# Kernel optimization log

Measured on AMD Instinct MI355X. Metric: run time of the kernel, lower is better.

Reference implementation:

```python
import jax, jax.numpy as jnp
import numpy as np

HEAD_NUM = 16
MASK_FILL = 100000.0  # source uses +1e5 on masked entries (not -inf)


def setup_inputs() -> dict:
    key = jax.random.key(0)
    k1, k2, k3, k4, k5 = jax.random.split(key, 5)
    B, S, E = 2, 2048, 1024
    scale = 0.02
    return {
        "x": jax.random.normal(k1, (B, S, E), dtype=jnp.float32),
        "W_atten": jax.random.normal(k2, (E, 3 * E), dtype=jnp.float32) * scale,
        "b_atten": jax.random.normal(k3, (3 * E,), dtype=jnp.float32) * scale,
        "W_proj": jax.random.normal(k4, (E, E), dtype=jnp.float32) * scale,
        "b_proj": jax.random.normal(k5, (E,), dtype=jnp.float32) * scale,
    }


def reference(x, W_atten, b_atten, W_proj, b_proj):
    B, S, E = x.shape
    H = HEAD_NUM
    hd = E // H
    # QKV projection: [B, S, 3E]
    qkv = x @ W_atten + b_atten
    # reshape [B, S, H, 3*hd] -> [B, H, S, 3*hd], chunk into q,k,v [B,H,S,hd]
    qkv = jnp.transpose(qkv.reshape(B, S, H, 3 * hd), (0, 2, 1, 3))
    q, k, v = jnp.split(qkv, 3, axis=-1)
    # raw scores, NO 1/sqrt(dk) scaling (faithful to source)
    w = jnp.einsum("bhqd,bhkd->bhqk", q, k)
    # causal mask applied as w*mask + (1-mask)*1e5 (faithful to source)
    mask = jnp.tril(jnp.ones((S, S), dtype=w.dtype))
    w = w * mask + (1.0 - mask) * MASK_FILL
    # softmax over dim=1 == HEAD axis (faithful to source quirk)
    w = jax.nn.softmax(w, axis=1)
    # attn_drop: identity in eval mode
    a = jnp.einsum("bhqk,bhkd->bhqd", w, v)  # [B,H,S,hd]
    a = jnp.transpose(a, (0, 2, 1, 3)).reshape(B, S, E)
    h = a @ W_proj + b_proj
    # resi_drop: identity in eval mode
    return h
```

## Files before the change

### kernel.cpp

```cpp
#include <hip/hip_runtime.h>

#define DI __device__ __forceinline__

typedef __attribute__((ext_vector_type(8))) short s16x8;
typedef __attribute__((ext_vector_type(4))) short s16x4;
typedef __attribute__((ext_vector_type(4))) float f32x4;

DI unsigned short f2bf(float f){
  unsigned u = __float_as_uint(f);
  u = (u + 0x7FFFu + ((u >> 16) & 1u)) >> 16;
  return (unsigned short)u;
}
DI float bf2f(unsigned short h){
  return __uint_as_float(((unsigned)h) << 16);
}

DI void gll16(const void* g, void* l){
  __builtin_amdgcn_global_load_lds((const __attribute__((address_space(1))) void*)g,
                                   (__attribute__((address_space(3))) void*)l, 16, 0, 0);
}

__global__ void cvt_kernel(const float* __restrict__ in, unsigned short* __restrict__ out, int n8){
  int i = blockIdx.x * blockDim.x + threadIdx.x;
  if (i >= n8) return;
  const float4* p = (const float4*)in + (size_t)i * 2;
  float4 a = p[0], b = p[1];
  s16x8 o;
  o[0] = (short)f2bf(a.x); o[1] = (short)f2bf(a.y); o[2] = (short)f2bf(a.z); o[3] = (short)f2bf(a.w);
  o[4] = (short)f2bf(b.x); o[5] = (short)f2bf(b.y); o[6] = (short)f2bf(b.z); o[7] = (short)f2bf(b.w);
  ((s16x8*)out)[i] = o;
}

__global__ void transpose_cvt(const float* __restrict__ in, unsigned short* __restrict__ out, int R, int C){
  __shared__ float t[32][33];
  int c0 = blockIdx.x * 32, r0 = blockIdx.y * 32;
  int tx = threadIdx.x, ty = threadIdx.y;
  #pragma unroll
  for (int i = 0; i < 4; i++)
    t[ty + i*8][tx] = in[(size_t)(r0 + ty + i*8) * C + c0 + tx];
  __syncthreads();
  #pragma unroll
  for (int i = 0; i < 4; i++)
    out[(size_t)(c0 + ty + i*8) * R + r0 + tx] = f2bf(t[tx][ty + i*8]);
}

template<int MODE>
__global__ void gemm_kernel(const unsigned short* __restrict__ A,
                            const unsigned short* __restrict__ Wt,
                            const float* __restrict__ bias,
                            int N,
                            unsigned short* __restrict__ qb,
                            unsigned short* __restrict__ kb,
                            unsigned short* __restrict__ vt,
                            float* __restrict__ out)
{
  const int K = 1024;
  __shared__ unsigned short As[128 * 72];
  __shared__ unsigned short Bs[128 * 72];
  int m0 = blockIdx.y * 128, n0 = blockIdx.x * 128;
  int tid = threadIdx.x;
  int lane = tid & 63, wid = tid >> 6;
  int wm = (wid >> 1) * 64, wn = (wid & 1) * 64;
  int row_l = lane & 15, kgrp = lane >> 4;

  f32x4 acc[4][4];
  #pragma unroll
  for (int i = 0; i < 4; i++)
    #pragma unroll
    for (int j = 0; j < 4; j++)
      acc[i][j] = (f32x4){0.f, 0.f, 0.f, 0.f};

  for (int k0 = 0; k0 < K; k0 += 64){
    #pragma unroll
    for (int i = 0; i < 4; i++){
      int cid = tid + i * 256;
      int r = cid >> 3, c = (cid & 7) * 8;
      *(s16x8*)&As[r * 72 + c] = *(const s16x8*)&A [(size_t)(m0 + r) * K + k0 + c];
      *(s16x8*)&Bs[r * 72 + c] = *(const s16x8*)&Wt[(size_t)(n0 + r) * K + k0 + c];
    }
    __syncthreads();
    #pragma unroll
    for (int kc = 0; kc < 2; kc++){
      s16x8 af[4], bfr[4];
      #pragma unroll
      for (int mi = 0; mi < 4; mi++)
        af[mi] = *(const s16x8*)&As[(wm + mi*16 + row_l) * 72 + kc*32 + kgrp*8];
      #pragma unroll
      for (int ni = 0; ni < 4; ni++)
        bfr[ni] = *(const s16x8*)&Bs[(wn + ni*16 + row_l) * 72 + kc*32 + kgrp*8];
      #pragma unroll
      for (int mi = 0; mi < 4; mi++)
        #pragma unroll
        for (int ni = 0; ni < 4; ni++)
          acc[mi][ni] = __builtin_amdgcn_mfma_f32_16x16x32_bf16(af[mi], bfr[ni], acc[mi][ni], 0, 0, 0);
    }
    __syncthreads();
  }

  #pragma unroll
  for (int mi = 0; mi < 4; mi++){
    #pragma unroll
    for (int ni = 0; ni < 4; ni++){
      #pragma unroll
      for (int j = 0; j < 4; j++){
        int gr = m0 + wm + mi*16 + kgrp*4 + j;
        int gc = n0 + wn + ni*16 + row_l;
        float v = acc[mi][ni][j] + bias[gc];
        if (MODE == 0){
          int h = gc / 192, cc = gc % 192;
          int b = gr >> 11, s = gr & 2047;
          unsigned short bv = f2bf(v);
          if (cc < 64){
            qb[(size_t)gr * 1024 + h*64 + cc] = bv;
          } else if (cc < 128){
            int d = cc - 64; int kt = s >> 6, kk = s & 63;
            kb[(size_t)((b*16 + h)*32 + kt) * 4096 + ((kk*64 + d) ^ ((kk & 7) << 3))] = bv;
          } else {
            int d = cc - 128; int kt = s >> 6, kk = s & 63;
            vt[(size_t)((b*16 + h)*32 + kt) * 4096 + ((d*64 + kk) ^ ((d & 7) << 3))] = bv;
          }
        } else {
          out[(size_t)gr * N + gc] = v;
        }
      }
    }
  }
}

__global__ void sufv_kernel(const unsigned short* __restrict__ vt, float* __restrict__ sufv){
  __shared__ float tot[4][64];
  int bh = blockIdx.x;
  int tid = threadIdx.x;
  int tq = tid >> 6, d = tid & 63;
  const unsigned short* base = vt + (size_t)bh * 32 * 4096;
  float s[8];
  float run = 0.f;
  for (int j = 7; j >= 0; j--){
    int t = tq*8 + j;
    float rs = 0.f;
    #pragma unroll
    for (int c = 0; c < 8; c++){
      int idx = (d*64 + c*8) ^ ((d & 7) << 3);
      s16x8 v = *(const s16x8*)&base[(size_t)t*4096 + idx];
      #pragma unroll
      for (int e = 0; e < 8; e++) rs += bf2f((unsigned short)v[e]);
    }
    run += rs; s[j] = run;
  }
  tot[tq][d] = run;
  __syncthreads();
  float carry = 0.f;
  for (int t2 = tq+1; t2 < 4; t2++) carry += tot[t2][d];
  #pragma unroll
  for (int j = 0; j < 8; j++)
    sufv[((size_t)bh*33 + tq*8 + j)*64 + d] = s[j] + carry;
  if (tid < 64) sufv[((size_t)bh*33 + 32)*64 + tid] = 0.f;
}

__launch_bounds__(256)
__global__ void dpass_kernel(const unsigned short* __restrict__ qbuf,
                             const unsigned short* __restrict__ kb,
                             float* __restrict__ invDT)
{
  __shared__ unsigned short Kst[2][4096];
  int blk = blockIdx.x;
  int b = blk / 528, t = blk % 528;
  int qt = (int)((sqrtf(8.f*t + 1.f) - 1.f) * 0.5f);
  while ((qt+1)*(qt+2)/2 <= t) qt++;
  while (qt*(qt+1)/2 > t) qt--;
  int kt = t - qt*(qt+1)/2;

  int tid = threadIdx.x, lane = tid & 63, w = tid >> 6;
  int row_l = lane & 15, kgrp = lane >> 4;

  const unsigned short* ktb = kb + ((size_t)(b*16)*32 + kt) * 4096;

  auto stage = [&](int h, int buf){
    const unsigned short* src = ktb + (size_t)h * 32 * 4096;
    #pragma unroll
    for (int c = 0; c < 2; c++)
      gll16(src + (w*128 + c*64 + lane)*8, (void*)(&Kst[buf][0] + w*1024 + c*512));
  };

  stage(0, 0);

  f32x4 esum[4];
  #pragma unroll
  for (int ks = 0; ks < 4; ks++) esum[ks] = (f32x4){0.f,0.f,0.f,0.f};

  const unsigned short* qrow_p = qbuf + (size_t)(b*2048 + qt*64 + w*16 + row_l) * 1024;
  s16x8 qf0 = *(const s16x8*)&qrow_p[kgrp*8];
  s16x8 qf1 = *(const s16x8*)&qrow_p[32 + kgrp*8];

  for (int h = 0; h < 16; h++){
    int buf = h & 1;
    s16x8 qn0, qn1;
    if (h < 15){
      qn0 = *(const s16x8*)&qrow_p[(h+1)*64 + kgrp*8];
      qn1 = *(const s16x8*)&qrow_p[(h+1)*64 + 32 + kgrp*8];
      stage(h+1, buf ^ 1);
    }
    __builtin_amdgcn_sched_barrier(0);
    if (h < 15) asm volatile("s_waitcnt vmcnt(4)" ::: "memory");
    else        asm volatile("s_waitcnt vmcnt(0)" ::: "memory");
    __builtin_amdgcn_sched_barrier(0);
    __builtin_amdgcn_s_barrier();
    __builtin_amdgcn_sched_barrier(0);

    #pragma unroll
    for (int ks = 0; ks < 4; ks++){
      int row = ks*16 + row_l;
      int e0 = (row*64 + kgrp*8) ^ ((row & 7) << 3);
      int e1 = (row*64 + 32 + kgrp*8) ^ ((row & 7) << 3);
      s16x8 a0 = *(const s16x8*)&Kst[buf][e0];
      s16x8 a1 = *(const s16x8*)&Kst[buf][e1];
      f32x4 sc = __builtin_amdgcn_mfma_f32_16x16x32_bf16(a0, qf0, (f32x4){0.f,0.f,0.f,0.f}, 0, 0, 0);
      sc = __builtin_amdgcn_mfma_f32_16x16x32_bf16(a1, qf1, sc, 0, 0, 0);
      #pragma unroll
      for (int j = 0; j < 4; j++) esum[ks][j] += __expf(sc[j]);
    }
    __builtin_amdgcn_sched_barrier(0);
    __builtin_amdgcn_s_barrier();
    if (h < 15){ qf0 = qn0; qf1 = qn1; }
  }

  int qcol = qt*64 + w*16 + row_l;
  #pragma unroll
  for (int ks = 0; ks < 4; ks++)
    #pragma unroll
    for (int j = 0; j < 4; j++){
      int key = kt*64 + ks*16 + kgrp*4 + j;
      invDT[(size_t)b*4194304 + (size_t)key*2048 + qcol] = 1.f / esum[ks][j];
    }
}

__launch_bounds__(256)
__global__ void pv_kernel(const unsigned short* __restrict__ qbuf,
                          const unsigned short* __restrict__ kb,
                          const unsigned short* __restrict__ vt,
                          const float* __restrict__ invDT,
                          const float* __restrict__ sufv,
                          unsigned short* __restrict__ ab,
                          float* __restrict__ pb)
{
  __shared__ unsigned short Kst[2][4096];
  __shared__ unsigned short Vst[2][4096];
  __shared__ unsigned short Ws[4][16*72];

  int blk = blockIdx.x;
  int b = blk >> 9;
  int r = blk & 511;
  int h = r >> 5;
  int r2 = r & 31;
  int i = r2 >> 1, half = r2 & 1;
  int qsm = i, qbig = 31 - i;

  int tid = threadIdx.x, lane = tid & 63, w = tid >> 6;
  int row_l = lane & 15, kgrp = lane >> 4;

  const unsigned short* KT = kb + (size_t)((b*16 + h)*32) * 4096;
  const unsigned short* VT = vt + (size_t)((b*16 + h)*32) * 4096;
  const float* invB = invDT + (size_t)b * 4194304;

  auto stage = [&](int kt, int par){
    #pragma unroll
    for (int c = 0; c < 2; c++){
      gll16(KT + (size_t)kt*4096 + (w*128 + c*64 + lane)*8, (void*)(&Kst[par][0] + w*1024 + c*512));
      gll16(VT + (size_t)kt*4096 + (w*128 + c*64 + lane)*8, (void*)(&Vst[par][0] + w*1024 + c*512));
    }
  };

  auto run = [&](int qt, int k0t, int k1t, int mode){
    int q0 = qt * 64;
    int qv = q0 + w*16 + row_l;
    const unsigned short* qrow_p = qbuf + (size_t)(b*2048 + qv) * 1024 + h*64;
    s16x8 qf0 = *(const s16x8*)&qrow_p[kgrp*8];
    s16x8 qf1 = *(const s16x8*)&qrow_p[32 + kgrp*8];

    f32x4 pv[4];
    #pragma unroll
    for (int d = 0; d < 4; d++) pv[d] = (f32x4){0.f,0.f,0.f,0.f};

    stage(k0t, 0);

    for (int kt = k0t; kt < k1t; kt++){
      int par = (kt - k0t) & 1;
      float invd[4][4];
      #pragma unroll
      for (int ks = 0; ks < 4; ks++)
        #pragma unroll
        for (int j = 0; j < 4; j++){
          int key = kt*64 + ks*16 + kgrp*4 + j;
          invd[ks][j] = invB[(size_t)key*2048 + qv];
        }
      bool has_next = (kt + 1 < k1t);
      if (has_next) stage(kt+1, par ^ 1);
      __builtin_amdgcn_sched_barrier(0);
      if (has_next) asm volatile("s_waitcnt vmcnt(20)" ::: "memory");
      else          asm volatile("s_waitcnt vmcnt(16)" ::: "memory");
      __builtin_amdgcn_sched_barrier(0);
      __builtin_amdgcn_s_barrier();
      __builtin_amdgcn_sched_barrier(0);

      f32x4 sc[4];
      #pragma unroll
      for (int ks = 0; ks < 4; ks++){
        int row = ks*16 + row_l;
        int e0 = (row*64 + kgrp*8) ^ ((row & 7) << 3);
        int e1 = (row*64 + 32 + kgrp*8) ^ ((row & 7) << 3);
        s16x8 a0 = *(const s16x8*)&Kst[par][e0];
        s16x8 a1 = *(const s16x8*)&Kst[par][e1];
        sc[ks] = __builtin_amdgcn_mfma_f32_16x16x32_bf16(a0, qf0, (f32x4){0.f,0.f,0.f,0.f}, 0, 0, 0);
        sc[ks] = __builtin_amdgcn_mfma_f32_16x16x32_bf16(a1, qf1, sc[ks], 0, 0, 0);
      }
      #pragma unroll
      for (int ks = 0; ks < 4; ks++){
        #pragma unroll
        for (int j = 0; j < 4; j++){
          int key = kt*64 + ks*16 + kgrp*4 + j;
          float e = __expf(sc[ks][j]);
          sc[ks][j] = (key > qv) ? 0.0625f : e * invd[ks][j];
        }
        s16x4 pk;
        pk[0] = (short)f2bf(sc[ks][0]); pk[1] = (short)f2bf(sc[ks][1]);
        pk[2] = (short)f2bf(sc[ks][2]); pk[3] = (short)f2bf(sc[ks][3]);
        *(s16x4*)&Ws[w][row_l*72 + ks*16 + kgrp*4] = pk;
      }
      #pragma unroll
      for (int kc = 0; kc < 2; kc++){
        s16x8 af = *(const s16x8*)&Ws[w][row_l*72 + kc*32 + kgrp*8];
        #pragma unroll
        for (int dq = 0; dq < 4; dq++){
          int row = dq*16 + row_l;
          int ev = (row*64 + kc*32 + kgrp*8) ^ ((row & 7) << 3);
          s16x8 vf = *(const s16x8*)&Vst[par][ev];
          pv[dq] = __builtin_amdgcn_mfma_f32_16x16x32_bf16(af, vf, pv[dq], 0, 0, 0);
        }
      }
      __builtin_amdgcn_sched_barrier(0);
      __builtin_amdgcn_s_barrier();
    }

    if (mode == 0){
      int tsuf = qt + 1;
      #pragma unroll
      for (int dq = 0; dq < 4; dq++){
        int d = dq*16 + row_l;
        float suf = sufv[((size_t)(b*16 + h)*33 + tsuf)*64 + d];
        #pragma unroll
        for (int j = 0; j < 4; j++){
          int qo = q0 + w*16 + kgrp*4 + j;
          ab[(size_t)(b*2048 + qo)*1024 + h*64 + d] = f2bf(pv[dq][j] + 0.0625f * suf);
        }
      }
    } else {
      float* pr = pb + ((size_t)((b*16 + h)*16 + i)*2 + (mode - 1)) * 4096;
      #pragma unroll
      for (int dq = 0; dq < 4; dq++){
        int d = dq*16 + row_l;
        #pragma unroll
        for (int j = 0; j < 4; j++)
          pr[(w*16 + kgrp*4 + j)*64 + d] = pv[dq][j];
      }
    }
  };

  if (half == 0){
    run(qsm, 0, i + 1, 0);
    run(qbig, 0, 16 - i, 1);
  } else {
    run(qbig, 16 - i, 32 - i, 2);
  }
}

__global__ void reduce_kernel(const float* __restrict__ pb,
                              const float* __restrict__ sufv,
                              unsigned short* __restrict__ ab)
{
  int blk = blockIdx.x;
  int b = blk >> 8, rr = blk & 255;
  int h = rr >> 4, i = rr & 15;
  int qbig = 31 - i, tsuf = 32 - i;
  int t = threadIdx.x;
  int q = t >> 2, dbase = (t & 3) * 16;
  const float* p0 = pb + ((size_t)((b*16 + h)*16 + i)*2 + 0)*4096 + q*64 + dbase;
  const float* p1 = p0 + 4096;
  const float* sf = sufv + ((size_t)(b*16 + h)*33 + tsuf)*64 + dbase;
  unsigned short* op = ab + (size_t)(b*2048 + qbig*64 + q)*1024 + h*64 + dbase;
  #pragma unroll
  for (int e = 0; e < 4; e++){
    float4 a = *(const float4*)(p0 + e*4);
    float4 bb = *(const float4*)(p1 + e*4);
    float4 s = *(const float4*)(sf + e*4);
    unsigned short o[4];
    o[0] = f2bf(a.x + bb.x + 0.0625f * s.x);
    o[1] = f2bf(a.y + bb.y + 0.0625f * s.y);
    o[2] = f2bf(a.z + bb.z + 0.0625f * s.z);
    o[3] = f2bf(a.w + bb.w + 0.0625f * s.w);
    *(s16x4*)(op + e*4) = *(s16x4*)o;
  }
}

extern "C" void kernel_launch(void* const* d_in, const int* in_sizes, int n_in,
                              void* d_out, int out_size, void* d_ws, size_t ws_size,
                              hipStream_t stream) {
  (void)in_sizes; (void)n_in; (void)out_size; (void)ws_size;
  const float* x  = (const float*)d_in[0];
  const float* Wa = (const float*)d_in[1];
  const float* ba = (const float*)d_in[2];
  const float* Wp = (const float*)d_in[3];
  const float* bp = (const float*)d_in[4];
  float* out = (float*)d_out;

  char* ws = (char*)d_ws;
  size_t off = 0;
  auto alloc = [&](size_t bytes) -> void* {
    void* p = ws + off;
    off += (bytes + 255) & ~(size_t)255;
    return p;
  };
  float* pbuf          = (float*)alloc((size_t)16*1024*1024);
  unsigned short* xb   = (unsigned short*)((char*)pbuf);
  unsigned short* WaT  = (unsigned short*)((char*)pbuf + (size_t)4096*1024*2);
  unsigned short* WpT  = (unsigned short*)alloc((size_t)1024*1024*2);
  unsigned short* qbuf = (unsigned short*)alloc((size_t)4096*1024*2);
  unsigned short* ktile= (unsigned short*)alloc((size_t)4096*1024*2);
  unsigned short* vtile= (unsigned short*)alloc((size_t)4096*1024*2);
  unsigned short* abuf = (unsigned short*)alloc((size_t)4096*1024*2);
  float* invDT         = (float*)alloc((size_t)2*2048*2048*4);
  float* sufv          = (float*)alloc((size_t)32*33*64*4);

  cvt_kernel<<<2048, 256, 0, stream>>>(x, xb, 4096*1024/8);
  transpose_cvt<<<dim3(3072/32, 1024/32), dim3(32, 8), 0, stream>>>(Wa, WaT, 1024, 3072);
  transpose_cvt<<<dim3(1024/32, 1024/32), dim3(32, 8), 0, stream>>>(Wp, WpT, 1024, 1024);

  gemm_kernel<0><<<dim3(24, 32), 256, 0, stream>>>(xb, WaT, ba, 3072, qbuf, ktile, vtile, nullptr);

  sufv_kernel<<<32, 256, 0, stream>>>(vtile, sufv);

  dpass_kernel<<<1056, 256, 0, stream>>>(qbuf, ktile, invDT);

  pv_kernel<<<1024, 256, 0, stream>>>(qbuf, ktile, vtile, invDT, sufv, abuf, pbuf);

  reduce_kernel<<<512, 256, 0, stream>>>(pbuf, sufv, abuf);

  gemm_kernel<1><<<dim3(8, 32), 256, 0, stream>>>(abuf, WpT, bp, 1024, nullptr, nullptr, nullptr, out);
}
```

Measured before the change: 177.8 us.

## Deepen K/V prefetch, use direct-to-LDS GEMM loads, and transpose the inverse-denominator layout

The GEMM now loads tiles with global_load_lds into XOR-swizzled unpadded LDS, instead of staging them through registers. The dpass and pv kernels move from double to quad buffering with a prefetch distance of two tiles, which lets them drop the trailing barrier in each iteration. The inverse-denominator buffer is stored query-major, so dpass writes it and pv reads it as float4 vectors, and pv prefetches the next tile's values. The pv kernel also uses v_cvt_pk_bf16_f32 for packing and dynamic shared memory. These changes aim to hide global latency and cut strided scalar traffic, at the cost of more LDS use and hand-tuned vmcnt counts that must stay exact.

Result: no change. 177.7 us (-0.1%).

```diff
diff --git a/kernel.cpp b/kernel.cpp
--- a/kernel.cpp
+++ b/kernel.cpp
@@ -45,6 +45,7 @@
 }
 
 template<int MODE>
+__launch_bounds__(256)
 __global__ void gemm_kernel(const unsigned short* __restrict__ A,
                             const unsigned short* __restrict__ Wt,
                             const float* __restrict__ bias,
@@ -55,13 +56,33 @@
                             float* __restrict__ out)
 {
   const int K = 1024;
-  __shared__ unsigned short As[128 * 72];
-  __shared__ unsigned short Bs[128 * 72];
+  __shared__ unsigned short As[128 * 64];
+  __shared__ unsigned short Bs[128 * 64];
   int m0 = blockIdx.y * 128, n0 = blockIdx.x * 128;
   int tid = threadIdx.x;
-  int lane = tid & 63, wid = tid >> 6;
-  int wm = (wid >> 1) * 64, wn = (wid & 1) * 64;
+  int lane = tid & 63, w = tid >> 6;
   int row_l = lane & 15, kgrp = lane >> 4;
+  int wm = (w >> 1) * 64, wn = (w & 1) * 64;
+
+  const unsigned short* asrc[4];
+  const unsigned short* bsrc[4];
+  int ldso[4];
+  int chunk = (lane & 7) ^ (lane >> 3);
+  #pragma unroll
+  for (int c4 = 0; c4 < 4; c4++){
+    int r = c4*32 + w*8 + (lane >> 3);
+    asrc[c4] = A  + (size_t)(m0 + r) * K + chunk*8;
+    bsrc[c4] = Wt + (size_t)(n0 + r) * K + chunk*8;
+    ldso[c4] = (c4*32 + w*8) * 64;
+  }
+  int eA[4], eB[4];
+  #pragma unroll
+  for (int i = 0; i < 4; i++){
+    int ra = wm + i*16 + row_l;
+    eA[i] = (ra*64 + kgrp*8) ^ ((ra & 7) << 3);
+    int rb = wn + i*16 + row_l;
+    eB[i] = (rb*64 + kgrp*8) ^ ((rb & 7) << 3);
+  }
 
   f32x4 acc[4][4];
   #pragma unroll
@@ -72,11 +93,9 @@
 
   for (int k0 = 0; k0 < K; k0 += 64){
     #pragma unroll
-    for (int i = 0; i < 4; i++){
-      int cid = tid + i * 256;
-      int r = cid >> 3, c = (cid & 7) * 8;
-      *(s16x8*)&As[r * 72 + c] = *(const s16x8*)&A [(size_t)(m0 + r) * K + k0 + c];
-      *(s16x8*)&Bs[r * 72 + c] = *(const s16x8*)&Wt[(size_t)(n0 + r) * K + k0 + c];
+    for (int c4 = 0; c4 < 4; c4++){
+      gll16(asrc[c4] + k0, (void*)(As + ldso[c4]));
+      gll16(bsrc[c4] + k0, (void*)(Bs + ldso[c4]));
     }
     __syncthreads();
     #pragma unroll
@@ -84,10 +103,10 @@
       s16x8 af[4], bfr[4];
       #pragma unroll
       for (int mi = 0; mi < 4; mi++)
-        af[mi] = *(const s16x8*)&As[(wm + mi*16 + row_l) * 72 + kc*32 + kgrp*8];
+        af[mi] = *(const s16x8*)&As[eA[mi] ^ (kc*32)];
       #pragma unroll
       for (int ni = 0; ni < 4; ni++)
-        bfr[ni] = *(const s16x8*)&Bs[(wn + ni*16 + row_l) * 72 + kc*32 + kgrp*8];
+        bfr[ni] = *(const s16x8*)&Bs[eB[ni] ^ (kc*32)];
       #pragma unroll
       for (int mi = 0; mi < 4; mi++)
         #pragma unroll
@@ -160,9 +179,9 @@
 __launch_bounds__(256)
 __global__ void dpass_kernel(const unsigned short* __restrict__ qbuf,
                              const unsigned short* __restrict__ kb,
-                             float* __restrict__ invDT)
+                             float* __restrict__ invDQ)
 {
-  __shared__ unsigned short Kst[2][4096];
+  __shared__ unsigned short Kst[4][4096];
   int blk = blockIdx.x;
   int b = blk / 528, t = blk % 528;
   int qt = (int)((sqrtf(8.f*t + 1.f) - 1.f) * 0.5f);
@@ -174,15 +193,23 @@
   int row_l = lane & 15, kgrp = lane >> 4;
 
   const unsigned short* ktb = kb + ((size_t)(b*16)*32 + kt) * 4096;
-
-  auto stage = [&](int h, int buf){
-    const unsigned short* src = ktb + (size_t)h * 32 * 4096;
-    #pragma unroll
-    for (int c = 0; c < 2; c++)
-      gll16(src + (w*128 + c*64 + lane)*8, (void*)(&Kst[buf][0] + w*1024 + c*512));
+  int sgoff = (w*128 + lane)*8;
+
+  auto stage = [&](int hh, int buf){
+    const unsigned short* src = ktb + (size_t)hh * 131072;
+    gll16(src + sgoff,       (void*)(&Kst[buf][0] + w*1024));
+    gll16(src + sgoff + 512, (void*)(&Kst[buf][0] + w*1024 + 512));
   };
 
+  int e0[4];
+  #pragma unroll
+  for (int ks = 0; ks < 4; ks++){
+    int row = ks*16 + row_l;
+    e0[ks] = (row*64 + kgrp*8) ^ ((row & 7) << 3);
+  }
+
   stage(0, 0);
+  stage(1, 1);
 
   f32x4 esum[4];
   #pragma unroll
@@ -193,59 +220,57 @@
   s16x8 qf1 = *(const s16x8*)&qrow_p[32 + kgrp*8];
 
   for (int h = 0; h < 16; h++){
-    int buf = h & 1;
     s16x8 qn0, qn1;
     if (h < 15){
       qn0 = *(const s16x8*)&qrow_p[(h+1)*64 + kgrp*8];
       qn1 = *(const s16x8*)&qrow_p[(h+1)*64 + 32 + kgrp*8];
-      stage(h+1, buf ^ 1);
-    }
+    }
+    if (h + 2 < 16) stage(h+2, (h+2) & 3);
     __builtin_amdgcn_sched_barrier(0);
-    if (h < 15) asm volatile("s_waitcnt vmcnt(4)" ::: "memory");
-    else        asm volatile("s_waitcnt vmcnt(0)" ::: "memory");
+    if (h < 14)      asm volatile("s_waitcnt vmcnt(8)" ::: "memory");
+    else if (h < 15) asm volatile("s_waitcnt vmcnt(6)" ::: "memory");
+    else             asm volatile("s_waitcnt vmcnt(2)" ::: "memory");
     __builtin_amdgcn_sched_barrier(0);
     __builtin_amdgcn_s_barrier();
     __builtin_amdgcn_sched_barrier(0);
 
+    const unsigned short* kl = &Kst[h & 3][0];
     #pragma unroll
     for (int ks = 0; ks < 4; ks++){
-      int row = ks*16 + row_l;
-      int e0 = (row*64 + kgrp*8) ^ ((row & 7) << 3);
-      int e1 = (row*64 + 32 + kgrp*8) ^ ((row & 7) << 3);
-      s16x8 a0 = *(const s16x8*)&Kst[buf][e0];
-      s16x8 a1 = *(const s16x8*)&Kst[buf][e1];
+      s16x8 a0 = *(const s16x8*)&kl[e0[ks]];
+      s16x8 a1 = *(const s16x8*)&kl[e0[ks] ^ 32];
       f32x4 sc = __builtin_amdgcn_mfma_f32_16x16x32_bf16(a0, qf0, (f32x4){0.f,0.f,0.f,0.f}, 0, 0, 0);
       sc = __builtin_amdgcn_mfma_f32_16x16x32_bf16(a1, qf1, sc, 0, 0, 0);
       #pragma unroll
       for (int j = 0; j < 4; j++) esum[ks][j] += __expf(sc[j]);
     }
-    __builtin_amdgcn_sched_barrier(0);
-    __builtin_amdgcn_s_barrier();
     if (h < 15){ qf0 = qn0; qf1 = qn1; }
   }
 
   int qcol = qt*64 + w*16 + row_l;
-  #pragma unroll
-  for (int ks = 0; ks < 4; ks++)
-    #pragma unroll
-    for (int j = 0; j < 4; j++){
-      int key = kt*64 + ks*16 + kgrp*4 + j;
-      invDT[(size_t)b*4194304 + (size_t)key*2048 + qcol] = 1.f / esum[ks][j];
-    }
+  float* dst = invDQ + (size_t)b*4194304 + (size_t)qcol*2048 + kt*64 + kgrp*4;
+  #pragma unroll
+  for (int ks = 0; ks < 4; ks++){
+    f32x4 rv;
+    #pragma unroll
+    for (int j = 0; j < 4; j++) rv[j] = 1.f / esum[ks][j];
+    *(f32x4*)&dst[ks*16] = rv;
+  }
 }
 
 __launch_bounds__(256)
 __global__ void pv_kernel(const unsigned short* __restrict__ qbuf,
                           const unsigned short* __restrict__ kb,
                           const unsigned short* __restrict__ vt,
-                          const float* __restrict__ invDT,
+                          const float* __restrict__ invDQ,
                           const float* __restrict__ sufv,
                           unsigned short* __restrict__ ab,
                           float* __restrict__ pb)
 {
-  __shared__ unsigned short Kst[2][4096];
-  __shared__ unsigned short Vst[2][4096];
-  __shared__ unsigned short Ws[4][16*72];
+  extern __shared__ unsigned short lds[];
+  unsigned short* KstB = lds;
+  unsigned short* VstB = lds + 16384;
+  unsigned short* WsB  = lds + 32768;
 
   int blk = blockIdx.x;
   int b = blk >> 9;
@@ -260,14 +285,21 @@
 
   const unsigned short* KT = kb + (size_t)((b*16 + h)*32) * 4096;
   const unsigned short* VT = vt + (size_t)((b*16 + h)*32) * 4096;
-  const float* invB = invDT + (size_t)b * 4194304;
-
-  auto stage = [&](int kt, int par){
-    #pragma unroll
-    for (int c = 0; c < 2; c++){
-      gll16(KT + (size_t)kt*4096 + (w*128 + c*64 + lane)*8, (void*)(&Kst[par][0] + w*1024 + c*512));
-      gll16(VT + (size_t)kt*4096 + (w*128 + c*64 + lane)*8, (void*)(&Vst[par][0] + w*1024 + c*512));
-    }
+  int sgoff = (w*128 + lane)*8;
+  unsigned short* Wsw = WsB + w*1152;
+
+  int eK[4];
+  #pragma unroll
+  for (int ks = 0; ks < 4; ks++){
+    int row = ks*16 + row_l;
+    eK[ks] = (row*64 + kgrp*8) ^ ((row & 7) << 3);
+  }
+
+  auto stage = [&](int kt, int buf){
+    gll16(KT + (size_t)kt*4096 + sgoff,       (void*)(KstB + buf*4096 + w*1024));
+    gll16(KT + (size_t)kt*4096 + sgoff + 512, (void*)(KstB + buf*4096 + w*1024 + 512));
+    gll16(VT + (size_t)kt*4096 + sgoff,       (void*)(VstB + buf*4096 + w*1024));
+    gll16(VT + (size_t)kt*4096 + sgoff + 512, (void*)(VstB + buf*4096 + w*1024 + 512));
   };
 
   auto run = [&](int qt, int k0t, int k1t, int mode){
@@ -276,69 +308,69 @@
     const unsigned short* qrow_p = qbuf + (size_t)(b*2048 + qv) * 1024 + h*64;
     s16x8 qf0 = *(const s16x8*)&qrow_p[kgrp*8];
     s16x8 qf1 = *(const s16x8*)&qrow_p[32 + kgrp*8];
-
-    f32x4 pv[4];
-    #pragma unroll
-    for (int d = 0; d < 4; d++) pv[d] = (f32x4){0.f,0.f,0.f,0.f};
+    const float* ivrow = invDQ + (size_t)b*4194304 + (size_t)qv*2048 + kgrp*4;
+
+    f32x4 pvv[4];
+    #pragma unroll
+    for (int d = 0; d < 4; d++) pvv[d] = (f32x4){0.f,0.f,0.f,0.f};
 
     stage(k0t, 0);
+    f32x4 inxt[4];
+    #pragma unroll
+    for (int ks = 0; ks < 4; ks++) inxt[ks] = *(const f32x4*)&ivrow[k0t*64 + ks*16];
+    if (k0t + 1 < k1t) stage(k0t+1, 1);
 
     for (int kt = k0t; kt < k1t; kt++){
-      int par = (kt - k0t) & 1;
-      float invd[4][4];
-      #pragma unroll
-      for (int ks = 0; ks < 4; ks++)
-        #pragma unroll
-        for (int j = 0; j < 4; j++){
-          int key = kt*64 + ks*16 + kgrp*4 + j;
-          invd[ks][j] = invB[(size_t)key*2048 + qv];
-        }
-      bool has_next = (kt + 1 < k1t);
-      if (has_next) stage(kt+1, par ^ 1);
+      int par = (kt - k0t) & 3;
+      f32x4 icur[4];
+      #pragma unroll
+      for (int ks = 0; ks < 4; ks++) icur[ks] = inxt[ks];
+      if (kt + 1 < k1t){
+        #pragma unroll
+        for (int ks = 0; ks < 4; ks++) inxt[ks] = *(const f32x4*)&ivrow[(kt+1)*64 + ks*16];
+      }
+      if (kt + 2 < k1t) stage(kt+2, (par + 2) & 3);
       __builtin_amdgcn_sched_barrier(0);
-      if (has_next) asm volatile("s_waitcnt vmcnt(20)" ::: "memory");
-      else          asm volatile("s_waitcnt vmcnt(16)" ::: "memory");
+      if (kt + 2 < k1t)      asm volatile("s_waitcnt vmcnt(16)" ::: "memory");
+      else if (kt + 1 < k1t) asm volatile("s_waitcnt vmcnt(12)" ::: "memory");
+      else                   asm volatile("s_waitcnt vmcnt(4)" ::: "memory");
       __builtin_amdgcn_sched_barrier(0);
       __builtin_amdgcn_s_barrier();
       __builtin_amdgcn_sched_barrier(0);
 
+      const unsigned short* kl = KstB + par*4096;
+      const unsigned short* vl = VstB + par*4096;
       f32x4 sc[4];
       #pragma unroll
       for (int ks = 0; ks < 4; ks++){
-        int row = ks*16 + row_l;
-        int e0 = (row*64 + kgrp*8) ^ ((row & 7) << 3);
-        int e1 = (row*64 + 32 + kgrp*8) ^ ((row & 7) << 3);
-        s16x8 a0 = *(const s16x8*)&Kst[par][e0];
-        s16x8 a1 = *(const s16x8*)&Kst[par][e1];
+        s16x8 a0 = *(const s16x8*)&kl[eK[ks]];
+        s16x8 a1 = *(const s16x8*)&kl[eK[ks] ^ 32];
         sc[ks] = __builtin_amdgcn_mfma_f32_16x16x32_bf16(a0, qf0, (f32x4){0.f,0.f,0.f,0.f}, 0, 0, 0);
         sc[ks] = __builtin_amdgcn_mfma_f32_16x16x32_bf16(a1, qf1, sc[ks], 0, 0, 0);
       }
+      int kbase = kt*64 + kgrp*4;
       #pragma unroll
       for (int ks = 0; ks < 4; ks++){
         #pragma unroll
         for (int j = 0; j < 4; j++){
-          int key = kt*64 + ks*16 + kgrp*4 + j;
           float e = __expf(sc[ks][j]);
-          sc[ks][j] = (key > qv) ? 0.0625f : e * invd[ks][j];
+          sc[ks][j] = (kbase + ks*16 + j > qv) ? 0.0625f : e * icur[ks][j];
         }
-        s16x4 pk;
-        pk[0] = (short)f2bf(sc[ks][0]); pk[1] = (short)f2bf(sc[ks][1]);
-        pk[2] = (short)f2bf(sc[ks][2]); pk[3] = (short)f2bf(sc[ks][3]);
-        *(s16x4*)&Ws[w][row_l*72 + ks*16 + kgrp*4] = pk;
+        unsigned lo, hi;
+        asm("v_cvt_pk_bf16_f32 %0, %1, %2" : "=v"(lo) : "v"(sc[ks][0]), "v"(sc[ks][1]));
+        asm("v_cvt_pk_bf16_f32 %0, %1, %2" : "=v"(hi) : "v"(sc[ks][2]), "v"(sc[ks][3]));
+        uint2 pk2; pk2.x = lo; pk2.y = hi;
+        *(uint2*)&Wsw[row_l*72 + ks*16 + kgrp*4] = pk2;
       }
       #pragma unroll
       for (int kc = 0; kc < 2; kc++){
-        s16x8 af = *(const s16x8*)&Ws[w][row_l*72 + kc*32 + kgrp*8];
+        s16x8 af = *(const s16x8*)&Wsw[row_l*72 + kc*32 + kgrp*8];
         #pragma unroll
         for (int dq = 0; dq < 4; dq++){
-          int row = dq*16 + row_l;
-          int ev = (row*64 + kc*32 + kgrp*8) ^ ((row & 7) << 3);
-          s16x8 vf = *(const s16x8*)&Vst[par][ev];
-          pv[dq] = __builtin_amdgcn_mfma_f32_16x16x32_bf16(af, vf, pv[dq], 0, 0, 0);
+          s16x8 vf = *(const s16x8*)&vl[eK[dq] ^ (kc*32)];
+          pvv[dq] = __builtin_amdgcn_mfma_f32_16x16x32_bf16(af, vf, pvv[dq], 0, 0, 0);
         }
       }
-      __builtin_amdgcn_sched_barrier(0);
-      __builtin_amdgcn_s_barrier();
     }
 
     if (mode == 0){
@@ -350,7 +382,7 @@
         #pragma unroll
         for (int j = 0; j < 4; j++){
           int qo = q0 + w*16 + kgrp*4 + j;
-          ab[(size_t)(b*2048 + qo)*1024 + h*64 + d] = f2bf(pv[dq][j] + 0.0625f * suf);
+          ab[(size_t)(b*2048 + qo)*1024 + h*64 + d] = f2bf(pvv[dq][j] + 0.0625f * suf);
         }
       }
     } else {
@@ -360,7 +392,7 @@
         int d = dq*16 + row_l;
         #pragma unroll
         for (int j = 0; j < 4; j++)
-          pr[(w*16 + kgrp*4 + j)*64 + d] = pv[dq][j];
+          pr[(w*16 + kgrp*4 + j)*64 + d] = pvv[dq][j];
       }
     }
   };
@@ -427,7 +459,7 @@
   unsigned short* ktile= (unsigned short*)alloc((size_t)4096*1024*2);
   unsigned short* vtile= (unsigned short*)alloc((size_t)4096*1024*2);
   unsigned short* abuf = (unsigned short*)alloc((size_t)4096*1024*2);
-  float* invDT         = (float*)alloc((size_t)2*2048*2048*4);
+  float* invDQ         = (float*)alloc((size_t)2*2048*2048*4);
   float* sufv          = (float*)alloc((size_t)32*33*64*4);
 
   cvt_kernel<<<2048, 256, 0, stream>>>(x, xb, 4096*1024/8);
@@ -438,9 +470,16 @@
 
   sufv_kernel<<<32, 256, 0, stream>>>(vtile, sufv);
 
-  dpass_kernel<<<1056, 256, 0, stream>>>(qbuf, ktile, invDT);
-
-  pv_kernel<<<1024, 256, 0, stream>>>(qbuf, ktile, vtile, invDT, sufv, abuf, pbuf);
+  dpass_kernel<<<1056, 256, 0, stream>>>(qbuf, ktile, invDQ);
+
+  static int smem_set = 0;
+  size_t smem = (size_t)(16384 + 16384 + 4608) * sizeof(unsigned short);
+  if (!smem_set) {
+    hipFuncSetAttribute(reinterpret_cast<const void*>(pv_kernel),
+                        hipFuncAttributeMaxDynamicSharedMemorySize, (int)smem);
+    smem_set = 1;
+  }
+  pv_kernel<<<1024, 256, smem, stream>>>(qbuf, ktile, vtile, invDQ, sufv, abuf, pbuf);
 
   reduce_kernel<<<512, 256, 0, stream>>>(pbuf, sufv, abuf);
 
```
